# Kernel optimization log

Measured on AMD Instinct MI355X. Metric: run time of the kernel, lower is better.

## Reference

```python
import jax, jax.numpy as jnp
import numpy as np

N_HEAD = 16
TEMPERATURE = 1.0

def setup_inputs() -> dict:
    key = jax.random.key(0)
    ks = jax.random.split(key, 5)
    B, L, D = 2, 2048, 1024
    s = 0.02
    return {
        'x':     jax.random.normal(ks[0], (B, L, D), jnp.float32),
        'q_g':   jax.random.normal(ks[1], (B, L, D), jnp.float32),
        'k_g':   jax.random.normal(ks[2], (B, L, D), jnp.float32),
        'W_qkv': jax.random.normal(ks[3], (D, 3 * D), jnp.float32) * s,
        'W_out': jax.random.normal(ks[4], (D, D), jnp.float32) * s,
    }

def reference(x, q_g, k_g, W_qkv, W_out):
    B, L, D = x.shape
    H = N_HEAD
    hd = D // H
    qkv = x @ W_qkv                                    # [B, L, 3D]
    q, k, v = jnp.split(qkv, 3, axis=-1)
    def to_heads(t):                                    # [B,L,D] -> [B,H,L,hd]
        return t.reshape(B, L, H, hd).transpose(0, 2, 1, 3)
    q, k, v = to_heads(q), to_heads(k), to_heads(v)
    qg, kg = to_heads(q_g), to_heads(k_g)

    scale = 1.0 / jnp.sqrt(jnp.float32(hd))
    # dual score matrices (same math as concat-on-head-dim then split)
    aw_x = jnp.einsum('bhqd,bhkd->bhqk', q, k) * scale    # [B,H,L,L]
    aw_g = jnp.einsum('bhqd,bhkd->bhqk', qg, kg) * scale  # [B,H,L,L]
    # sensory_attention=True, merge='add'
    attn = aw_x + aw_g

    causal = jnp.tril(jnp.ones((L, L), dtype=bool))
    attn = jnp.where(causal, attn, -jnp.inf)
    log_norm = jnp.log(jnp.float32(L))                    # softmax_log_norm=True
    attn = jax.nn.softmax(attn / (log_norm * TEMPERATURE), axis=-1)

    y = jnp.einsum('bhqk,bhkd->bhqd', attn, v)            # [B,H,L,hd]
    y = y.transpose(0, 2, 1, 3).reshape(B, L, D)
    return y @ W_out
```

## Files before the change

### kernel.cpp

```cpp
#include <hip/hip_runtime.h>

typedef __attribute__((ext_vector_type(8))) short bf16x8;
typedef __attribute__((ext_vector_type(4))) float f32x4;

static __device__ __forceinline__ unsigned short f2bf(float f) {
    unsigned int u = __float_as_uint(f);
    u += 0x7fffu + ((u >> 16) & 1u);
    return (unsigned short)(u >> 16);
}
static __device__ __forceinline__ unsigned int pack2bf(float lo, float hi) {
    return ((__float_as_uint(lo) + 0x8000u) >> 16) |
           ((__float_as_uint(hi) + 0x8000u) & 0xffff0000u);
}
static __device__ __forceinline__ float bf2f(short v) {
    return __uint_as_float(((unsigned int)(unsigned short)v) << 16);
}
static __device__ __forceinline__ bf16x8 cvt8v(const float* p) {
    f32x4 a = *(const f32x4*)p, b = *(const f32x4*)(p + 4);
    bf16x8 r;
    r[0] = (short)f2bf(a[0]); r[1] = (short)f2bf(a[1]);
    r[2] = (short)f2bf(a[2]); r[3] = (short)f2bf(a[3]);
    r[4] = (short)f2bf(b[0]); r[5] = (short)f2bf(b[1]);
    r[6] = (short)f2bf(b[2]); r[7] = (short)f2bf(b[3]);
    return r;
}
static __device__ __forceinline__ bf16x8 scale8v(bf16x8 v, float s) {
    bf16x8 r;
    #pragma unroll
    for (int j = 0; j < 8; ++j) r[j] = (short)f2bf(bf2f(v[j]) * s);
    return r;
}
static __device__ __forceinline__ uint4 cvt8(const float* p) {
    bf16x8 r = cvt8v(p);
    union { bf16x8 v; uint4 u; } c; c.v = r; return c.u;
}
static __device__ __forceinline__ void glds16(const unsigned short* g, unsigned short* l) {
    __builtin_amdgcn_global_load_lds(
        (const __attribute__((address_space(1))) unsigned int*)g,
        (__attribute__((address_space(3))) unsigned int*)l, 16, 0, 0);
}

static __device__ __forceinline__ void transpose_tile(
    const float* __restrict__ src, unsigned short* __restrict__ dst,
    int R, int C, int bx, int by, int tid)
{
    __shared__ unsigned short t[64 * 72];
    const int r0 = by * 64, c0 = bx * 64;
    #pragma unroll
    for (int i = 0; i < 4; ++i) {
        int idx = tid + i * 256;
        int row = idx >> 4, seg = idx & 15;
        f32x4 v = *(const f32x4*)&src[(size_t)(r0 + row) * C + c0 + seg * 4];
        #pragma unroll
        for (int j = 0; j < 4; ++j) t[row * 72 + seg * 4 + j] = f2bf(v[j]);
    }
    __syncthreads();
    #pragma unroll
    for (int i = 0; i < 2; ++i) {
        int idx = tid + i * 256;
        int row = idx >> 3, seg = idx & 7;
        uint4 tv; unsigned short* tmp = (unsigned short*)&tv;
        #pragma unroll
        for (int j = 0; j < 8; ++j) tmp[j] = t[(seg * 8 + j) * 72 + row];
        *(uint4*)&dst[(size_t)(c0 + row) * R + r0 + seg * 8] = tv;
    }
}

__global__ __launch_bounds__(256) void prep_all(
    const float* __restrict__ x, unsigned short* __restrict__ x_bf,
    const float* __restrict__ kg, unsigned short* __restrict__ kg_bf,
    const float* __restrict__ Wq, unsigned short* __restrict__ wtq,
    const float* __restrict__ Wo, unsigned short* __restrict__ wto)
{
    const int t = blockIdx.x, tid = threadIdx.x;
    if (t < 2048) {
        size_t j = ((size_t)t * 256 + tid) * 8;
        *(uint4*)&x_bf[j] = cvt8(&x[j]);
    } else if (t < 4096) {
        size_t j = ((size_t)(t - 2048) * 256 + tid) * 8;
        *(uint4*)&kg_bf[j] = cvt8(&kg[j]);
    } else if (t < 4864) {
        int tt = t - 4096;
        transpose_tile(Wq, wtq, 1024, 3072, tt % 48, tt / 48, tid);
    } else {
        int tt = t - 4864;
        transpose_tile(Wo, wto, 1024, 1024, tt & 15, tt >> 4, tid);
    }
}

__global__ __launch_bounds__(256) void gemm_qkv(
    const unsigned short* __restrict__ A, const unsigned short* __restrict__ Bt,
    unsigned short* __restrict__ qk, unsigned short* __restrict__ vt)
{
    const int K = 1024;
    __shared__ unsigned short As[128 * 32];
    __shared__ unsigned short Bs[128 * 32];
    __shared__ unsigned short Tb[128 * 136];
    const int tid = threadIdx.x;
    const int wave = tid >> 6, lane = tid & 63, quad = lane >> 4, l16 = lane & 15;
    const int wr = (wave >> 1) * 64, wc = (wave & 1) * 64;
    const int m0 = blockIdx.y * 128, n0 = blockIdx.x * 128;

    const unsigned short* ga = A  + (size_t)(m0 + wave * 32 + (lane >> 2)) * K + (lane & 3) * 8;
    const unsigned short* gb = Bt + (size_t)(n0 + wave * 32 + (lane >> 2)) * K + (lane & 3) * 8;
    unsigned short* la = &As[wave * 32 * 32];
    unsigned short* lb = &Bs[wave * 32 * 32];
    const size_t step16 = (size_t)16 * K;

    f32x4 acc[4][4];
    #pragma unroll
    for (int i = 0; i < 4; ++i)
        #pragma unroll
        for (int j = 0; j < 4; ++j) acc[i][j] = (f32x4){0.f, 0.f, 0.f, 0.f};

    for (int kt = 0; kt < K; kt += 32) {
        glds16(ga, la); glds16(ga + step16, la + 512);
        glds16(gb, lb); glds16(gb + step16, lb + 512);
        ga += 32; gb += 32;
        __syncthreads();
        bf16x8 af[4], bf[4];
        #pragma unroll
        for (int i = 0; i < 4; ++i) {
            af[i] = *(const bf16x8*)&As[(wr + i * 16 + l16) * 32 + quad * 8];
            bf[i] = *(const bf16x8*)&Bs[(wc + i * 16 + l16) * 32 + quad * 8];
        }
        #pragma unroll
        for (int mi = 0; mi < 4; ++mi)
            #pragma unroll
            for (int ni = 0; ni < 4; ++ni)
                acc[mi][ni] = __builtin_amdgcn_mfma_f32_16x16x32_bf16(
                    af[mi], bf[ni], acc[mi][ni], 0, 0, 0);
        __syncthreads();
    }

    if (blockIdx.x < 16) {
        #pragma unroll
        for (int mi = 0; mi < 4; ++mi)
            #pragma unroll
            for (int ni = 0; ni < 4; ++ni)
                #pragma unroll
                for (int r = 0; r < 4; ++r) {
                    int row = m0 + wr + mi * 16 + quad * 4 + r;
                    int col = n0 + wc + ni * 16 + l16;
                    qk[(size_t)row * 2048 + col] = f2bf(acc[mi][ni][r]);
                }
    } else {
        __syncthreads();
        #pragma unroll
        for (int mi = 0; mi < 4; ++mi)
            #pragma unroll
            for (int ni = 0; ni < 4; ++ni)
                #pragma unroll
                for (int r = 0; r < 4; ++r) {
                    int col = wc + ni * 16 + l16;
                    int row = wr + mi * 16 + quad * 4 + r;
                    Tb[col * 136 + row] = f2bf(acc[mi][ni][r]);
                }
        __syncthreads();
        const int col = tid >> 1, r0 = (tid & 1) * 64;
        const int bh = (m0 >> 11) * 16 + ((int)blockIdx.x - 16) * 2 + (col >> 6);
        size_t base = ((size_t)bh * 64 + (col & 63)) * 2048 + (m0 & 2047) + r0;
        #pragma unroll
        for (int k = 0; k < 8; ++k)
            *(uint4*)&vt[base + k * 8] = *(const uint4*)&Tb[col * 136 + r0 + k * 8];
    }
}

__global__ __launch_bounds__(256) void gemm_n64(
    const unsigned short* __restrict__ A, const unsigned short* __restrict__ Bt,
    float* __restrict__ C)
{
    const int K = 1024, N = 1024;
    __shared__ unsigned short As[128 * 32];
    __shared__ unsigned short Bs[64 * 32];
    const int tid = threadIdx.x;
    const int wave = tid >> 6, lane = tid & 63, quad = lane >> 4, l16 = lane & 15;
    const int wr = (wave >> 1) * 64, wc = (wave & 1) * 32;
    const int m0 = blockIdx.y * 128, n0 = blockIdx.x * 64;

    const unsigned short* ga = A  + (size_t)(m0 + wave * 32 + (lane >> 2)) * K + (lane & 3) * 8;
    const unsigned short* gb = Bt + (size_t)(n0 + wave * 16 + (lane >> 2)) * K + (lane & 3) * 8;
    unsigned short* la = &As[wave * 32 * 32];
    unsigned short* lb = &Bs[wave * 16 * 32];
    const size_t step16 = (size_t)16 * K;

    f32x4 acc[4][2];
    #pragma unroll
    for (int i = 0; i < 4; ++i)
        #pragma unroll
        for (int j = 0; j < 2; ++j) acc[i][j] = (f32x4){0.f, 0.f, 0.f, 0.f};

    for (int kt = 0; kt < K; kt += 32) {
        glds16(ga, la); glds16(ga + step16, la + 512);
        glds16(gb, lb);
        ga += 32; gb += 32;
        __syncthreads();
        bf16x8 af[4], bf[2];
        #pragma unroll
        for (int i = 0; i < 4; ++i)
            af[i] = *(const bf16x8*)&As[(wr + i * 16 + l16) * 32 + quad * 8];
        #pragma unroll
        for (int i = 0; i < 2; ++i)
            bf[i] = *(const bf16x8*)&Bs[(wc + i * 16 + l16) * 32 + quad * 8];
        #pragma unroll
        for (int mi = 0; mi < 4; ++mi)
            #pragma unroll
            for (int ni = 0; ni < 2; ++ni)
                acc[mi][ni] = __builtin_amdgcn_mfma_f32_16x16x32_bf16(
                    af[mi], bf[ni], acc[mi][ni], 0, 0, 0);
        __syncthreads();
    }
    #pragma unroll
    for (int mi = 0; mi < 4; ++mi)
        #pragma unroll
        for (int ni = 0; ni < 2; ++ni)
            #pragma unroll
            for (int r = 0; r < 4; ++r) {
                int row = m0 + wr + mi * 16 + quad * 4 + r;
                int col = n0 + wc + ni * 16 + l16;
                C[(size_t)row * N + col] = acc[mi][ni][r];
            }
}

__global__ __launch_bounds__(256, 5) void attn7(
    const unsigned short* __restrict__ qk, const float* __restrict__ qg,
    const unsigned short* __restrict__ kgb, const unsigned short* __restrict__ vt,
    unsigned short* __restrict__ y)
{
    const int L = 2048, DS = 2048, Dm = 1024;
    const float SC2 = 0.125f * 1.44269504088896f / 7.6246189861593985f;

    const int qt = 31 - (int)blockIdx.y;
    const int bh = blockIdx.x, b = bh >> 4, h = bh & 15;
    const int tid = threadIdx.x, wave = tid >> 6, lane = tid & 63;
    const int quad = lane >> 4, l16 = lane & 15;

    __shared__ unsigned short K_l[4096];
    __shared__ unsigned short G_l[4096];
    __shared__ unsigned short V_l[4096];
    __shared__ unsigned short P_l[4096];
    unsigned short* Pw = &P_l[wave * 1024];

    bf16x8 qf[2], gf[2];
    {
        const int qrow = qt * 64 + wave * 16 + l16;
        const unsigned short* qp = qk + (size_t)(b * L + qrow) * DS + h * 64;
        const float* gp = qg + (size_t)(b * L + qrow) * Dm + h * 64;
        #pragma unroll
        for (int c = 0; c < 2; ++c) {
            qf[c] = scale8v(*(const bf16x8*)(qp + c * 32 + quad * 8), SC2);
            gf[c] = scale8v(cvt8v(gp + c * 32 + quad * 8), SC2);
        }
    }

    f32x4 o[4];
    #pragma unroll
    for (int nd = 0; nd < 4; ++nd) o[nd] = (f32x4){0.f, 0.f, 0.f, 0.f};
    float lsum = 0.f;

    const int srow = wave * 16 + (lane >> 3);
    const int c8 = (((lane & 7) ^ (lane >> 3)) & 7) * 8;
    const unsigned short* pk = qk + (size_t)(b * L + srow) * DS + 1024 + h * 64 + c8;
    const unsigned short* pg = kgb + (size_t)(b * L + srow) * Dm + h * 64 + c8;
    const unsigned short* pv = vt + ((size_t)bh * 64 + srow) * L + c8;
    unsigned short* lK = &K_l[wave * 1024];
    unsigned short* lG = &G_l[wave * 1024];
    unsigned short* lV = &V_l[wave * 1024];

    const int rb = l16 * 128;
    const int swz0 = ((quad     ^ (l16 & 7)) * 16);
    const int swz1 = (((4 + quad) ^ (l16 & 7)) * 16);
    const int pwb = l16 * 64 + (quad & 1) * 4;
    const int pwc = quad >> 1, pxr = l16 & 7;

    for (int kt = 0; kt < qt; ++kt) {
        __syncthreads();
        glds16(pk, lK); glds16(pk + 8 * DS, lK + 512);
        glds16(pg, lG); glds16(pg + 8 * Dm, lG + 512);
        glds16(pv, lV); glds16(pv + 8 * L,  lV + 512);
        pk += 64 * DS; pg += 64 * Dm; pv += 64;
        __syncthreads();

        #pragma unroll
        for (int ni = 0; ni < 4; ++ni) {
            bf16x8 kf0 = *(const bf16x8*)((const char*)K_l + rb + swz0 + ni * 2048);
            bf16x8 kf1 = *(const bf16x8*)((const char*)K_l + rb + swz1 + ni * 2048);
            bf16x8 gb0 = *(const bf16x8*)((const char*)G_l + rb + swz0 + ni * 2048);
            bf16x8 gb1 = *(const bf16x8*)((const char*)G_l + rb + swz1 + ni * 2048);
            f32x4 a = (f32x4){0.f, 0.f, 0.f, 0.f};
            a = __builtin_amdgcn_mfma_f32_16x16x32_bf16(kf0, qf[0], a, 0, 0, 0);
            a = __builtin_amdgcn_mfma_f32_16x16x32_bf16(gb0, gf[0], a, 0, 0, 0);
            a = __builtin_amdgcn_mfma_f32_16x16x32_bf16(kf1, qf[1], a, 0, 0, 0);
            a = __builtin_amdgcn_mfma_f32_16x16x32_bf16(gb1, gf[1], a, 0, 0, 0);
            float e0 = exp2f(a[0]), e1 = exp2f(a[1]);
            float e2 = exp2f(a[2]), e3 = exp2f(a[3]);
            lsum += (e0 + e1) + (e2 + e3);
            unsigned int p01 = pack2bf(e0, e1), p23 = pack2bf(e2, e3);
            *(unsigned long long*)&Pw[pwb + (((ni * 2 + pwc) ^ pxr) * 8)] =
                ((unsigned long long)p23 << 32) | p01;
        }
        asm volatile("s_waitcnt lgkmcnt(0)" ::: "memory");

        bf16x8 pa[2];
        #pragma unroll
        for (int c = 0; c < 2; ++c)
            pa[c] = *(const bf16x8*)&Pw[l16 * 64 + (((c * 4 + quad) ^ pxr) * 8)];
        #pragma unroll
        for (int nd = 0; nd < 4; ++nd) {
            bf16x8 vf0 = *(const bf16x8*)((const char*)V_l + rb + swz0 + nd * 2048);
            bf16x8 vf1 = *(const bf16x8*)((const char*)V_l + rb + swz1 + nd * 2048);
            o[nd] = __builtin_amdgcn_mfma_f32_16x16x32_bf16(pa[0], vf0, o[nd], 0, 0, 0);
            o[nd] = __builtin_amdgcn_mfma_f32_16x16x32_bf16(pa[1], vf1, o[nd], 0, 0, 0);
        }
    }

    {
        __syncthreads();
        glds16(pk, lK); glds16(pk + 8 * DS, lK + 512);
        glds16(pg, lG); glds16(pg + 8 * Dm, lG + 512);
        glds16(pv, lV); glds16(pv + 8 * L,  lV + 512);
        __syncthreads();

        #pragma unroll
        for (int ni = 0; ni < 4; ++ni) {
            if (ni > wave) {
                *(unsigned long long*)&Pw[pwb + (((ni * 2 + pwc) ^ pxr) * 8)] = 0ull;
                continue;
            }
            bf16x8 kf0 = *(const bf16x8*)((const char*)K_l + rb + swz0 + ni * 2048);
            bf16x8 kf1 = *(const bf16x8*)((const char*)K_l + rb + swz1 + ni * 2048);
            bf16x8 gb0 = *(const bf16x8*)((const char*)G_l + rb + swz0 + ni * 2048);
            bf16x8 gb1 = *(const bf16x8*)((const char*)G_l + rb + swz1 + ni * 2048);
            f32x4 a = (f32x4){0.f, 0.f, 0.f, 0.f};
            a = __builtin_amdgcn_mfma_f32_16x16x32_bf16(kf0, qf[0], a, 0, 0, 0);
            a = __builtin_amdgcn_mfma_f32_16x16x32_bf16(gb0, gf[0], a, 0, 0, 0);
            a = __builtin_amdgcn_mfma_f32_16x16x32_bf16(kf1, qf[1], a, 0, 0, 0);
            a = __builtin_amdgcn_mfma_f32_16x16x32_bf16(gb1, gf[1], a, 0, 0, 0);
            float e0, e1, e2, e3;
            if (ni < wave) {
                e0 = exp2f(a[0]); e1 = exp2f(a[1]);
                e2 = exp2f(a[2]); e3 = exp2f(a[3]);
            } else {
                e0 = (quad * 4 + 0 <= l16) ? exp2f(a[0]) : 0.f;
                e1 = (quad * 4 + 1 <= l16) ? exp2f(a[1]) : 0.f;
                e2 = (quad * 4 + 2 <= l16) ? exp2f(a[2]) : 0.f;
                e3 = (quad * 4 + 3 <= l16) ? exp2f(a[3]) : 0.f;
            }
            lsum += (e0 + e1) + (e2 + e3);
            unsigned int p01 = pack2bf(e0, e1), p23 = pack2bf(e2, e3);
            *(unsigned long long*)&Pw[pwb + (((ni * 2 + pwc) ^ pxr) * 8)] =
                ((unsigned long long)p23 << 32) | p01;
        }
        asm volatile("s_waitcnt lgkmcnt(0)" ::: "memory");

        bf16x8 pa[2];
        #pragma unroll
        for (int c = 0; c < 2; ++c)
            pa[c] = *(const bf16x8*)&Pw[l16 * 64 + (((c * 4 + quad) ^ pxr) * 8)];
        #pragma unroll
        for (int nd = 0; nd < 4; ++nd) {
            bf16x8 vf0 = *(const bf16x8*)((const char*)V_l + rb + swz0 + nd * 2048);
            bf16x8 vf1 = *(const bf16x8*)((const char*)V_l + rb + swz1 + nd * 2048);
            o[nd] = __builtin_amdgcn_mfma_f32_16x16x32_bf16(pa[0], vf0, o[nd], 0, 0, 0);
            o[nd] = __builtin_amdgcn_mfma_f32_16x16x32_bf16(pa[1], vf1, o[nd], 0, 0, 0);
        }
    }

    float rs = lsum;
    rs += __shfl_xor(rs, 16);
    rs += __shfl_xor(rs, 32);
    #pragma unroll
    for (int r = 0; r < 4; ++r) {
        float inv = 1.f / __shfl(rs, (lane & 48) | (quad * 4 + r));
        int row = qt * 64 + wave * 16 + quad * 4 + r;
        #pragma unroll
        for (int nd = 0; nd < 4; ++nd)
            y[(size_t)(b * L + row) * Dm + h * 64 + nd * 16 + l16] =
                f2bf(o[nd][r] * inv);
    }
}

extern "C" void kernel_launch(void* const* d_in, const int* in_sizes, int n_in,
                              void* d_out, int out_size, void* d_ws, size_t ws_size,
                              hipStream_t stream) {
    const float* x     = (const float*)d_in[0];
    const float* q_g   = (const float*)d_in[1];
    const float* k_g   = (const float*)d_in[2];
    const float* W_qkv = (const float*)d_in[3];
    const float* W_out = (const float*)d_in[4];
    float* out = (float*)d_out;
    unsigned short* ws = (unsigned short*)d_ws;

    unsigned short* qk_ws = ws;
    unsigned short* y_ws  = ws + 8388608;
    unsigned short* wtq   = ws + 12582912;
    unsigned short* wto   = ws + 15728640;
    unsigned short* kg_bf = ws + 16777216;
    unsigned short* x_bf  = ws + 20971520;
    unsigned short* vt_bf = ws + 25165824;

    dim3 blk(256);
    prep_all<<<5120, blk, 0, stream>>>(x, x_bf, k_g, kg_bf, W_qkv, wtq, W_out, wto);
    gemm_qkv<<<dim3(24, 32), blk, 0, stream>>>(x_bf, wtq, qk_ws, vt_bf);
    attn7<<<dim3(32, 32), blk, 0, stream>>>(qk_ws, q_g, kg_bf, vt_bf, y_ws);
    gemm_n64<<<dim3(16, 32), blk, 0, stream>>>(y_ws, wto, out);
}
```

Measured before the change: 225.1 us.

## Double-buffer K/G/V tiles and widen attention query tile to 128 rows

Result: slower. 240.1 us (+6.7%).

```diff
diff --git a/kernel.cpp b/kernel.cpp
--- a/kernel.cpp
+++ b/kernel.cpp
@@ -222,7 +222,84 @@
             }
 }
 
-__global__ __launch_bounds__(256, 5) void attn7(
+template<bool DIAG>
+static __device__ __forceinline__ void attn_tile(
+    const unsigned short* __restrict__ Kc, const unsigned short* __restrict__ Gc,
+    const unsigned short* __restrict__ Vc, unsigned short* __restrict__ Pw,
+    const bf16x8 (&qf)[2][2], const bf16x8 (&gf)[2][2],
+    f32x4 (&o)[2][4], float (&lsum)[2],
+    int rb, int swz0, int swz1, int pxr, int quad, int l16, int wave, int reld)
+{
+    auto pstore = [&](int qj, int ni, unsigned long long v) {
+        *(unsigned long long*)&Pw[(qj * 16 + l16) * 64 + (quad & 1) * 4 +
+                                  (((ni * 2 + (quad >> 1)) ^ pxr) * 8)] = v;
+    };
+
+    #pragma unroll
+    for (int ni = 0; ni < 4; ++ni) {
+        const int kbase = (DIAG ? reld * 64 : 0) + ni * 16;
+        if (DIAG && kbase > wave * 32 + 31) {
+            pstore(0, ni, 0ull); pstore(1, ni, 0ull);
+            continue;
+        }
+        bf16x8 kf0 = *(const bf16x8*)((const char*)Kc + rb + swz0 + ni * 2048);
+        bf16x8 kf1 = *(const bf16x8*)((const char*)Kc + rb + swz1 + ni * 2048);
+        bf16x8 gb0 = *(const bf16x8*)((const char*)Gc + rb + swz0 + ni * 2048);
+        bf16x8 gb1 = *(const bf16x8*)((const char*)Gc + rb + swz1 + ni * 2048);
+        #pragma unroll
+        for (int qj = 0; qj < 2; ++qj) {
+            const int qtop = wave * 32 + qj * 16;
+            if (DIAG && kbase > qtop + 15) {
+                pstore(qj, ni, 0ull);
+                continue;
+            }
+            f32x4 a = (f32x4){0.f, 0.f, 0.f, 0.f};
+            a = __builtin_amdgcn_mfma_f32_16x16x32_bf16(kf0, qf[qj][0], a, 0, 0, 0);
+            a = __builtin_amdgcn_mfma_f32_16x16x32_bf16(gb0, gf[qj][0], a, 0, 0, 0);
+            a = __builtin_amdgcn_mfma_f32_16x16x32_bf16(kf1, qf[qj][1], a, 0, 0, 0);
+            a = __builtin_amdgcn_mfma_f32_16x16x32_bf16(gb1, gf[qj][1], a, 0, 0, 0);
+            float e0, e1, e2, e3;
+            if (DIAG && (kbase + 15 > qtop)) {
+                const int qr = qtop + l16, kb = kbase + quad * 4;
+                e0 = (kb + 0 <= qr) ? exp2f(a[0]) : 0.f;
+                e1 = (kb + 1 <= qr) ? exp2f(a[1]) : 0.f;
+                e2 = (kb + 2 <= qr) ? exp2f(a[2]) : 0.f;
+                e3 = (kb + 3 <= qr) ? exp2f(a[3]) : 0.f;
+            } else {
+                e0 = exp2f(a[0]); e1 = exp2f(a[1]);
+                e2 = exp2f(a[2]); e3 = exp2f(a[3]);
+            }
+            lsum[qj] += (e0 + e1) + (e2 + e3);
+            unsigned int p01 = pack2bf(e0, e1), p23 = pack2bf(e2, e3);
+            pstore(qj, ni, ((unsigned long long)p23 << 32) | p01);
+        }
+    }
+
+    bf16x8 vf[4][2];
+    #pragma unroll
+    for (int nd = 0; nd < 4; ++nd) {
+        vf[nd][0] = *(const bf16x8*)((const char*)Vc + rb + swz0 + nd * 2048);
+        vf[nd][1] = *(const bf16x8*)((const char*)Vc + rb + swz1 + nd * 2048);
+    }
+    asm volatile("s_waitcnt lgkmcnt(0)" ::: "memory");
+
+    bf16x8 pa[2][2];
+    #pragma unroll
+    for (int qj = 0; qj < 2; ++qj)
+        #pragma unroll
+        for (int c = 0; c < 2; ++c)
+            pa[qj][c] = *(const bf16x8*)&Pw[(qj * 16 + l16) * 64 +
+                                            (((c * 4 + quad) ^ pxr) * 8)];
+    #pragma unroll
+    for (int nd = 0; nd < 4; ++nd) {
+        o[0][nd] = __builtin_amdgcn_mfma_f32_16x16x32_bf16(pa[0][0], vf[nd][0], o[0][nd], 0, 0, 0);
+        o[0][nd] = __builtin_amdgcn_mfma_f32_16x16x32_bf16(pa[0][1], vf[nd][1], o[0][nd], 0, 0, 0);
+        o[1][nd] = __builtin_amdgcn_mfma_f32_16x16x32_bf16(pa[1][0], vf[nd][0], o[1][nd], 0, 0, 0);
+        o[1][nd] = __builtin_amdgcn_mfma_f32_16x16x32_bf16(pa[1][1], vf[nd][1], o[1][nd], 0, 0, 0);
+    }
+}
+
+__global__ __launch_bounds__(256, 2) void attn8(
     const unsigned short* __restrict__ qk, const float* __restrict__ qg,
     const unsigned short* __restrict__ kgb, const unsigned short* __restrict__ vt,
     unsigned short* __restrict__ y)
@@ -230,153 +307,96 @@
     const int L = 2048, DS = 2048, Dm = 1024;
     const float SC2 = 0.125f * 1.44269504088896f / 7.6246189861593985f;
 
-    const int qt = 31 - (int)blockIdx.y;
+    const int yb = (int)blockIdx.y;
+    const int qt = (yb < 8) ? (15 - yb) : (yb - 8);
     const int bh = blockIdx.x, b = bh >> 4, h = bh & 15;
     const int tid = threadIdx.x, wave = tid >> 6, lane = tid & 63;
     const int quad = lane >> 4, l16 = lane & 15;
 
-    __shared__ unsigned short K_l[4096];
-    __shared__ unsigned short G_l[4096];
-    __shared__ unsigned short V_l[4096];
-    __shared__ unsigned short P_l[4096];
-    unsigned short* Pw = &P_l[wave * 1024];
-
-    bf16x8 qf[2], gf[2];
-    {
-        const int qrow = qt * 64 + wave * 16 + l16;
-        const unsigned short* qp = qk + (size_t)(b * L + qrow) * DS + h * 64;
-        const float* gp = qg + (size_t)(b * L + qrow) * Dm + h * 64;
+    __shared__ unsigned short K_l[2][4096];
+    __shared__ unsigned short G_l[2][4096];
+    __shared__ unsigned short V_l[2][4096];
+    __shared__ unsigned short P_l[8192];
+    unsigned short* Pw = &P_l[wave * 2048];
+
+    bf16x8 qf[2][2], gf[2][2];
+    const int qrow0 = qt * 128 + wave * 32;
+    #pragma unroll
+    for (int qj = 0; qj < 2; ++qj) {
+        const unsigned short* qp = qk + (size_t)(b * L + qrow0 + qj * 16 + l16) * DS + h * 64;
+        const float* gp = qg + (size_t)(b * L + qrow0 + qj * 16 + l16) * Dm + h * 64;
         #pragma unroll
         for (int c = 0; c < 2; ++c) {
-            qf[c] = scale8v(*(const bf16x8*)(qp + c * 32 + quad * 8), SC2);
-            gf[c] = scale8v(cvt8v(gp + c * 32 + quad * 8), SC2);
+            qf[qj][c] = scale8v(*(const bf16x8*)(qp + c * 32 + quad * 8), SC2);
+            gf[qj][c] = scale8v(cvt8v(gp + c * 32 + quad * 8), SC2);
         }
     }
 
-    f32x4 o[4];
-    #pragma unroll
-    for (int nd = 0; nd < 4; ++nd) o[nd] = (f32x4){0.f, 0.f, 0.f, 0.f};
-    float lsum = 0.f;
+    f32x4 o[2][4];
+    #pragma unroll
+    for (int qj = 0; qj < 2; ++qj)
+        #pragma unroll
+        for (int nd = 0; nd < 4; ++nd) o[qj][nd] = (f32x4){0.f, 0.f, 0.f, 0.f};
+    float lsum[2] = {0.f, 0.f};
 
     const int srow = wave * 16 + (lane >> 3);
     const int c8 = (((lane & 7) ^ (lane >> 3)) & 7) * 8;
     const unsigned short* pk = qk + (size_t)(b * L + srow) * DS + 1024 + h * 64 + c8;
     const unsigned short* pg = kgb + (size_t)(b * L + srow) * Dm + h * 64 + c8;
     const unsigned short* pv = vt + ((size_t)bh * 64 + srow) * L + c8;
-    unsigned short* lK = &K_l[wave * 1024];
-    unsigned short* lG = &G_l[wave * 1024];
-    unsigned short* lV = &V_l[wave * 1024];
-
-    const int rb = l16 * 128;
-    const int swz0 = ((quad     ^ (l16 & 7)) * 16);
-    const int swz1 = (((4 + quad) ^ (l16 & 7)) * 16);
-    const int pwb = l16 * 64 + (quad & 1) * 4;
-    const int pwc = quad >> 1, pxr = l16 & 7;
-
-    for (int kt = 0; kt < qt; ++kt) {
-        __syncthreads();
+
+    auto STAGE = [&](int bi) {
+        unsigned short* lK = &K_l[bi][wave * 1024];
+        unsigned short* lG = &G_l[bi][wave * 1024];
+        unsigned short* lV = &V_l[bi][wave * 1024];
         glds16(pk, lK); glds16(pk + 8 * DS, lK + 512);
         glds16(pg, lG); glds16(pg + 8 * Dm, lG + 512);
         glds16(pv, lV); glds16(pv + 8 * L,  lV + 512);
         pk += 64 * DS; pg += 64 * Dm; pv += 64;
-        __syncthreads();
-
-        #pragma unroll
-        for (int ni = 0; ni < 4; ++ni) {
-            bf16x8 kf0 = *(const bf16x8*)((const char*)K_l + rb + swz0 + ni * 2048);
-            bf16x8 kf1 = *(const bf16x8*)((const char*)K_l + rb + swz1 + ni * 2048);
-            bf16x8 gb0 = *(const bf16x8*)((const char*)G_l + rb + swz0 + ni * 2048);
-            bf16x8 gb1 = *(const bf16x8*)((const char*)G_l + rb + swz1 + ni * 2048);
-            f32x4 a = (f32x4){0.f, 0.f, 0.f, 0.f};
-            a = __builtin_amdgcn_mfma_f32_16x16x32_bf16(kf0, qf[0], a, 0, 0, 0);
-            a = __builtin_amdgcn_mfma_f32_16x16x32_bf16(gb0, gf[0], a, 0, 0, 0);
-            a = __builtin_amdgcn_mfma_f32_16x16x32_bf16(kf1, qf[1], a, 0, 0, 0);
-            a = __builtin_amdgcn_mfma_f32_16x16x32_bf16(gb1, gf[1], a, 0, 0, 0);
-            float e0 = exp2f(a[0]), e1 = exp2f(a[1]);
-            float e2 = exp2f(a[2]), e3 = exp2f(a[3]);
-            lsum += (e0 + e1) + (e2 + e3);
-            unsigned int p01 = pack2bf(e0, e1), p23 = pack2bf(e2, e3);
-            *(unsigned long long*)&Pw[pwb + (((ni * 2 + pwc) ^ pxr) * 8)] =
-                ((unsigned long long)p23 << 32) | p01;
+    };
+
+    const int rb = l16 * 128;
+    const int swz0 = ((quad ^ (l16 & 7)) * 16);
+    const int swz1 = (((4 + quad) ^ (l16 & 7)) * 16);
+    const int pxr = l16 & 7;
+
+    STAGE(0);
+    int cur = 0;
+
+    for (int kt = 0; kt < 2 * qt; ++kt) {
+        asm volatile("s_waitcnt vmcnt(0)" ::: "memory");
+        __syncthreads();
+        STAGE(cur ^ 1);
+        attn_tile<false>(&K_l[cur][0], &G_l[cur][0], &V_l[cur][0], Pw,
+                         qf, gf, o, lsum, rb, swz0, swz1, pxr, quad, l16, wave, 0);
+        cur ^= 1;
+    }
+
+    #pragma unroll
+    for (int d = 0; d < 2; ++d) {
+        asm volatile("s_waitcnt vmcnt(0)" ::: "memory");
+        __syncthreads();
+        if (d == 0) STAGE(cur ^ 1);
+        if (!(d == 1 && wave < 2))
+            attn_tile<true>(&K_l[cur][0], &G_l[cur][0], &V_l[cur][0], Pw,
+                            qf, gf, o, lsum, rb, swz0, swz1, pxr, quad, l16, wave, d);
+        cur ^= 1;
+    }
+
+    #pragma unroll
+    for (int qj = 0; qj < 2; ++qj) {
+        float rs = lsum[qj];
+        rs += __shfl_xor(rs, 16);
+        rs += __shfl_xor(rs, 32);
+        #pragma unroll
+        for (int r = 0; r < 4; ++r) {
+            float inv = 1.f / __shfl(rs, (lane & 48) | (quad * 4 + r));
+            int row = qt * 128 + wave * 32 + qj * 16 + quad * 4 + r;
+            #pragma unroll
+            for (int nd = 0; nd < 4; ++nd)
+                y[(size_t)(b * L + row) * Dm + h * 64 + nd * 16 + l16] =
+                    f2bf(o[qj][nd][r] * inv);
         }
-        asm volatile("s_waitcnt lgkmcnt(0)" ::: "memory");
-
-        bf16x8 pa[2];
-        #pragma unroll
-        for (int c = 0; c < 2; ++c)
-            pa[c] = *(const bf16x8*)&Pw[l16 * 64 + (((c * 4 + quad) ^ pxr) * 8)];
-        #pragma unroll
-        for (int nd = 0; nd < 4; ++nd) {
-            bf16x8 vf0 = *(const bf16x8*)((const char*)V_l + rb + swz0 + nd * 2048);
-            bf16x8 vf1 = *(const bf16x8*)((const char*)V_l + rb + swz1 + nd * 2048);
-            o[nd] = __builtin_amdgcn_mfma_f32_16x16x32_bf16(pa[0], vf0, o[nd], 0, 0, 0);
-            o[nd] = __builtin_amdgcn_mfma_f32_16x16x32_bf16(pa[1], vf1, o[nd], 0, 0, 0);
-        }
-    }
-
-    {
-        __syncthreads();
-        glds16(pk, lK); glds16(pk + 8 * DS, lK + 512);
-        glds16(pg, lG); glds16(pg + 8 * Dm, lG + 512);
-        glds16(pv, lV); glds16(pv + 8 * L,  lV + 512);
-        __syncthreads();
-
-        #pragma unroll
-        for (int ni = 0; ni < 4; ++ni) {
-            if (ni > wave) {
-                *(unsigned long long*)&Pw[pwb + (((ni * 2 + pwc) ^ pxr) * 8)] = 0ull;
-                continue;
-            }
-            bf16x8 kf0 = *(const bf16x8*)((const char*)K_l + rb + swz0 + ni * 2048);
-            bf16x8 kf1 = *(const bf16x8*)((const char*)K_l + rb + swz1 + ni * 2048);
-            bf16x8 gb0 = *(const bf16x8*)((const char*)G_l + rb + swz0 + ni * 2048);
-            bf16x8 gb1 = *(const bf16x8*)((const char*)G_l + rb + swz1 + ni * 2048);
-            f32x4 a = (f32x4){0.f, 0.f, 0.f, 0.f};
-            a = __builtin_amdgcn_mfma_f32_16x16x32_bf16(kf0, qf[0], a, 0, 0, 0);
-            a = __builtin_amdgcn_mfma_f32_16x16x32_bf16(gb0, gf[0], a, 0, 0, 0);
-            a = __builtin_amdgcn_mfma_f32_16x16x32_bf16(kf1, qf[1], a, 0, 0, 0);
-            a = __builtin_amdgcn_mfma_f32_16x16x32_bf16(gb1, gf[1], a, 0, 0, 0);
-            float e0, e1, e2, e3;
-            if (ni < wave) {
-                e0 = exp2f(a[0]); e1 = exp2f(a[1]);
-                e2 = exp2f(a[2]); e3 = exp2f(a[3]);
-            } else {
-                e0 = (quad * 4 + 0 <= l16) ? exp2f(a[0]) : 0.f;
-                e1 = (quad * 4 + 1 <= l16) ? exp2f(a[1]) : 0.f;
-                e2 = (quad * 4 + 2 <= l16) ? exp2f(a[2]) : 0.f;
-                e3 = (quad * 4 + 3 <= l16) ? exp2f(a[3]) : 0.f;
-            }
-            lsum += (e0 + e1) + (e2 + e3);
-            unsigned int p01 = pack2bf(e0, e1), p23 = pack2bf(e2, e3);
-            *(unsigned long long*)&Pw[pwb + (((ni * 2 + pwc) ^ pxr) * 8)] =
-                ((unsigned long long)p23 << 32) | p01;
-        }
-        asm volatile("s_waitcnt lgkmcnt(0)" ::: "memory");
-
-        bf16x8 pa[2];
-        #pragma unroll
-        for (int c = 0; c < 2; ++c)
-            pa[c] = *(const bf16x8*)&Pw[l16 * 64 + (((c * 4 + quad) ^ pxr) * 8)];
-        #pragma unroll
-        for (int nd = 0; nd < 4; ++nd) {
-            bf16x8 vf0 = *(const bf16x8*)((const char*)V_l + rb + swz0 + nd * 2048);
-            bf16x8 vf1 = *(const bf16x8*)((const char*)V_l + rb + swz1 + nd * 2048);
-            o[nd] = __builtin_amdgcn_mfma_f32_16x16x32_bf16(pa[0], vf0, o[nd], 0, 0, 0);
-            o[nd] = __builtin_amdgcn_mfma_f32_16x16x32_bf16(pa[1], vf1, o[nd], 0, 0, 0);
-        }
-    }
-
-    float rs = lsum;
-    rs += __shfl_xor(rs, 16);
-    rs += __shfl_xor(rs, 32);
-    #pragma unroll
-    for (int r = 0; r < 4; ++r) {
-        float inv = 1.f / __shfl(rs, (lane & 48) | (quad * 4 + r));
-        int row = qt * 64 + wave * 16 + quad * 4 + r;
-        #pragma unroll
-        for (int nd = 0; nd < 4; ++nd)
-            y[(size_t)(b * L + row) * Dm + h * 64 + nd * 16 + l16] =
-                f2bf(o[nd][r] * inv);
     }
 }
 
@@ -402,6 +422,6 @@
     dim3 blk(256);
     prep_all<<<5120, blk, 0, stream>>>(x, x_bf, k_g, kg_bf, W_qkv, wtq, W_out, wto);
     gemm_qkv<<<dim3(24, 32), blk, 0, stream>>>(x_bf, wtq, qk_ws, vt_bf);
-    attn7<<<dim3(32, 32), blk, 0, stream>>>(qk_ws, q_g, kg_bf, vt_bf, y_ws);
+    attn8<<<dim3(32, 16), blk, 0, stream>>>(qk_ws, q_g, kg_bf, vt_bf, y_ws);
     gemm_n64<<<dim3(16, 32), blk, 0, stream>>>(y_ws, wto, out);
 }
```

## Double-buffer K/G/V LDS tiles in attention to overlap loads with compute

Applied to the files above, without the earlier changes.

After: 236.7 us. +5.1%, slower.

```diff
diff --git a/kernel.cpp b/kernel.cpp
--- a/kernel.cpp
+++ b/kernel.cpp
@@ -222,7 +222,66 @@
             }
 }
 
-__global__ __launch_bounds__(256, 5) void attn7(
+template<bool DIAG>
+static __device__ __forceinline__ void attn_tile(
+    const unsigned short* __restrict__ Kc, const unsigned short* __restrict__ Gc,
+    const unsigned short* __restrict__ Vc, unsigned short* __restrict__ Pw,
+    const bf16x8 (&qf)[2], const bf16x8 (&gf)[2],
+    f32x4 (&o)[4], float& lsum,
+    int rb, int swz0, int swz1, int pxr, int quad, int l16, int wave,
+    int pwb, int pwc)
+{
+    #pragma unroll
+    for (int ni = 0; ni < 4; ++ni) {
+        if (DIAG && ni > wave) {
+            *(unsigned long long*)&Pw[pwb + (((ni * 2 + pwc) ^ pxr) * 8)] = 0ull;
+            continue;
+        }
+        bf16x8 kf0 = *(const bf16x8*)((const char*)Kc + rb + swz0 + ni * 2048);
+        bf16x8 kf1 = *(const bf16x8*)((const char*)Kc + rb + swz1 + ni * 2048);
+        bf16x8 gb0 = *(const bf16x8*)((const char*)Gc + rb + swz0 + ni * 2048);
+        bf16x8 gb1 = *(const bf16x8*)((const char*)Gc + rb + swz1 + ni * 2048);
+        f32x4 a = (f32x4){0.f, 0.f, 0.f, 0.f};
+        a = __builtin_amdgcn_mfma_f32_16x16x32_bf16(kf0, qf[0], a, 0, 0, 0);
+        a = __builtin_amdgcn_mfma_f32_16x16x32_bf16(gb0, gf[0], a, 0, 0, 0);
+        a = __builtin_amdgcn_mfma_f32_16x16x32_bf16(kf1, qf[1], a, 0, 0, 0);
+        a = __builtin_amdgcn_mfma_f32_16x16x32_bf16(gb1, gf[1], a, 0, 0, 0);
+        float e0, e1, e2, e3;
+        if (DIAG && ni == wave) {
+            e0 = (quad * 4 + 0 <= l16) ? exp2f(a[0]) : 0.f;
+            e1 = (quad * 4 + 1 <= l16) ? exp2f(a[1]) : 0.f;
+            e2 = (quad * 4 + 2 <= l16) ? exp2f(a[2]) : 0.f;
+            e3 = (quad * 4 + 3 <= l16) ? exp2f(a[3]) : 0.f;
+        } else {
+            e0 = exp2f(a[0]); e1 = exp2f(a[1]);
+            e2 = exp2f(a[2]); e3 = exp2f(a[3]);
+        }
+        lsum += (e0 + e1) + (e2 + e3);
+        unsigned int p01 = pack2bf(e0, e1), p23 = pack2bf(e2, e3);
+        *(unsigned long long*)&Pw[pwb + (((ni * 2 + pwc) ^ pxr) * 8)] =
+            ((unsigned long long)p23 << 32) | p01;
+    }
+
+    bf16x8 vf[4][2];
+    #pragma unroll
+    for (int nd = 0; nd < 4; ++nd) {
+        vf[nd][0] = *(const bf16x8*)((const char*)Vc + rb + swz0 + nd * 2048);
+        vf[nd][1] = *(const bf16x8*)((const char*)Vc + rb + swz1 + nd * 2048);
+    }
+    asm volatile("s_waitcnt lgkmcnt(0)" ::: "memory");
+
+    bf16x8 pa[2];
+    #pragma unroll
+    for (int c = 0; c < 2; ++c)
+        pa[c] = *(const bf16x8*)&Pw[l16 * 64 + (((c * 4 + quad) ^ pxr) * 8)];
+    #pragma unroll
+    for (int nd = 0; nd < 4; ++nd) {
+        o[nd] = __builtin_amdgcn_mfma_f32_16x16x32_bf16(pa[0], vf[nd][0], o[nd], 0, 0, 0);
+        o[nd] = __builtin_amdgcn_mfma_f32_16x16x32_bf16(pa[1], vf[nd][1], o[nd], 0, 0, 0);
+    }
+}
+
+__global__ __launch_bounds__(256, 3) void attn10(
     const unsigned short* __restrict__ qk, const float* __restrict__ qg,
     const unsigned short* __restrict__ kgb, const unsigned short* __restrict__ vt,
     unsigned short* __restrict__ y)
@@ -235,9 +294,9 @@
     const int tid = threadIdx.x, wave = tid >> 6, lane = tid & 63;
     const int quad = lane >> 4, l16 = lane & 15;
 
-    __shared__ unsigned short K_l[4096];
-    __shared__ unsigned short G_l[4096];
-    __shared__ unsigned short V_l[4096];
+    __shared__ unsigned short K_l[2][4096];
+    __shared__ unsigned short G_l[2][4096];
+    __shared__ unsigned short V_l[2][4096];
     __shared__ unsigned short P_l[4096];
     unsigned short* Pw = &P_l[wave * 1024];
 
@@ -263,9 +322,16 @@
     const unsigned short* pk = qk + (size_t)(b * L + srow) * DS + 1024 + h * 64 + c8;
     const unsigned short* pg = kgb + (size_t)(b * L + srow) * Dm + h * 64 + c8;
     const unsigned short* pv = vt + ((size_t)bh * 64 + srow) * L + c8;
-    unsigned short* lK = &K_l[wave * 1024];
-    unsigned short* lG = &G_l[wave * 1024];
-    unsigned short* lV = &V_l[wave * 1024];
+
+    auto STAGE = [&](int bi) {
+        unsigned short* lK = &K_l[bi][wave * 1024];
+        unsigned short* lG = &G_l[bi][wave * 1024];
+        unsigned short* lV = &V_l[bi][wave * 1024];
+        glds16(pk, lK); glds16(pk + 8 * DS, lK + 512);
+        glds16(pg, lG); glds16(pg + 8 * Dm, lG + 512);
+        glds16(pv, lV); glds16(pv + 8 * L,  lV + 512);
+        pk += 64 * DS; pg += 64 * Dm; pv += 64;
+    };
 
     const int rb = l16 * 128;
     const int swz0 = ((quad     ^ (l16 & 7)) * 16);
@@ -273,97 +339,23 @@
     const int pwb = l16 * 64 + (quad & 1) * 4;
     const int pwc = quad >> 1, pxr = l16 & 7;
 
+    STAGE(0);
+    int cur = 0;
+
     for (int kt = 0; kt < qt; ++kt) {
         __syncthreads();
-        glds16(pk, lK); glds16(pk + 8 * DS, lK + 512);
-        glds16(pg, lG); glds16(pg + 8 * Dm, lG + 512);
-        glds16(pv, lV); glds16(pv + 8 * L,  lV + 512);
-        pk += 64 * DS; pg += 64 * Dm; pv += 64;
-        __syncthreads();
-
-        #pragma unroll
-        for (int ni = 0; ni < 4; ++ni) {
-            bf16x8 kf0 = *(const bf16x8*)((const char*)K_l + rb + swz0 + ni * 2048);
-            bf16x8 kf1 = *(const bf16x8*)((const char*)K_l + rb + swz1 + ni * 2048);
-            bf16x8 gb0 = *(const bf16x8*)((const char*)G_l + rb + swz0 + ni * 2048);
-            bf16x8 gb1 = *(const bf16x8*)((const char*)G_l + rb + swz1 + ni * 2048);
-            f32x4 a = (f32x4){0.f, 0.f, 0.f, 0.f};
-            a = __builtin_amdgcn_mfma_f32_16x16x32_bf16(kf0, qf[0], a, 0, 0, 0);
-            a = __builtin_amdgcn_mfma_f32_16x16x32_bf16(gb0, gf[0], a, 0, 0, 0);
-            a = __builtin_amdgcn_mfma_f32_16x16x32_bf16(kf1, qf[1], a, 0, 0, 0);
-            a = __builtin_amdgcn_mfma_f32_16x16x32_bf16(gb1, gf[1], a, 0, 0, 0);
-            float e0 = exp2f(a[0]), e1 = exp2f(a[1]);
-            float e2 = exp2f(a[2]), e3 = exp2f(a[3]);
-            lsum += (e0 + e1) + (e2 + e3);
-            unsigned int p01 = pack2bf(e0, e1), p23 = pack2bf(e2, e3);
-            *(unsigned long long*)&Pw[pwb + (((ni * 2 + pwc) ^ pxr) * 8)] =
-                ((unsigned long long)p23 << 32) | p01;
-        }
-        asm volatile("s_waitcnt lgkmcnt(0)" ::: "memory");
-
-        bf16x8 pa[2];
-        #pragma unroll
-        for (int c = 0; c < 2; ++c)
-            pa[c] = *(const bf16x8*)&Pw[l16 * 64 + (((c * 4 + quad) ^ pxr) * 8)];
-        #pragma unroll
-        for (int nd = 0; nd < 4; ++nd) {
-            bf16x8 vf0 = *(const bf16x8*)((const char*)V_l + rb + swz0 + nd * 2048);
-            bf16x8 vf1 = *(const bf16x8*)((const char*)V_l + rb + swz1 + nd * 2048);
-            o[nd] = __builtin_amdgcn_mfma_f32_16x16x32_bf16(pa[0], vf0, o[nd], 0, 0, 0);
-            o[nd] = __builtin_amdgcn_mfma_f32_16x16x32_bf16(pa[1], vf1, o[nd], 0, 0, 0);
-        }
+        STAGE(cur ^ 1);
+        attn_tile<false>(&K_l[cur][0], &G_l[cur][0], &V_l[cur][0], Pw,
+                         qf, gf, o, lsum, rb, swz0, swz1, pxr, quad, l16, wave,
+                         pwb, pwc);
+        cur ^= 1;
     }
 
     {
         __syncthreads();
-        glds16(pk, lK); glds16(pk + 8 * DS, lK + 512);
-        glds16(pg, lG); glds16(pg + 8 * Dm, lG + 512);
-        glds16(pv, lV); glds16(pv + 8 * L,  lV + 512);
-        __syncthreads();
-
-        #pragma unroll
-        for (int ni = 0; ni < 4; ++ni) {
-            if (ni > wave) {
-                *(unsigned long long*)&Pw[pwb + (((ni * 2 + pwc) ^ pxr) * 8)] = 0ull;
-                continue;
-            }
-            bf16x8 kf0 = *(const bf16x8*)((const char*)K_l + rb + swz0 + ni * 2048);
-            bf16x8 kf1 = *(const bf16x8*)((const char*)K_l + rb + swz1 + ni * 2048);
-            bf16x8 gb0 = *(const bf16x8*)((const char*)G_l + rb + swz0 + ni * 2048);
-            bf16x8 gb1 = *(const bf16x8*)((const char*)G_l + rb + swz1 + ni * 2048);
-            f32x4 a = (f32x4){0.f, 0.f, 0.f, 0.f};
-            a = __builtin_amdgcn_mfma_f32_16x16x32_bf16(kf0, qf[0], a, 0, 0, 0);
-            a = __builtin_amdgcn_mfma_f32_16x16x32_bf16(gb0, gf[0], a, 0, 0, 0);
-            a = __builtin_amdgcn_mfma_f32_16x16x32_bf16(kf1, qf[1], a, 0, 0, 0);
-            a = __builtin_amdgcn_mfma_f32_16x16x32_bf16(gb1, gf[1], a, 0, 0, 0);
-            float e0, e1, e2, e3;
-            if (ni < wave) {
-                e0 = exp2f(a[0]); e1 = exp2f(a[1]);
-                e2 = exp2f(a[2]); e3 = exp2f(a[3]);
-            } else {
-                e0 = (quad * 4 + 0 <= l16) ? exp2f(a[0]) : 0.f;
-                e1 = (quad * 4 + 1 <= l16) ? exp2f(a[1]) : 0.f;
-                e2 = (quad * 4 + 2 <= l16) ? exp2f(a[2]) : 0.f;
-                e3 = (quad * 4 + 3 <= l16) ? exp2f(a[3]) : 0.f;
-            }
-            lsum += (e0 + e1) + (e2 + e3);
-            unsigned int p01 = pack2bf(e0, e1), p23 = pack2bf(e2, e3);
-            *(unsigned long long*)&Pw[pwb + (((ni * 2 + pwc) ^ pxr) * 8)] =
-                ((unsigned long long)p23 << 32) | p01;
-        }
-        asm volatile("s_waitcnt lgkmcnt(0)" ::: "memory");
-
-        bf16x8 pa[2];
-        #pragma unroll
-        for (int c = 0; c < 2; ++c)
-            pa[c] = *(const bf16x8*)&Pw[l16 * 64 + (((c * 4 + quad) ^ pxr) * 8)];
-        #pragma unroll
-        for (int nd = 0; nd < 4; ++nd) {
-            bf16x8 vf0 = *(const bf16x8*)((const char*)V_l + rb + swz0 + nd * 2048);
-            bf16x8 vf1 = *(const bf16x8*)((const char*)V_l + rb + swz1 + nd * 2048);
-            o[nd] = __builtin_amdgcn_mfma_f32_16x16x32_bf16(pa[0], vf0, o[nd], 0, 0, 0);
-            o[nd] = __builtin_amdgcn_mfma_f32_16x16x32_bf16(pa[1], vf1, o[nd], 0, 0, 0);
-        }
+        attn_tile<true>(&K_l[cur][0], &G_l[cur][0], &V_l[cur][0], Pw,
+                        qf, gf, o, lsum, rb, swz0, swz1, pxr, quad, l16, wave,
+                        pwb, pwc);
     }
 
     float rs = lsum;
@@ -402,6 +394,6 @@
     dim3 blk(256);
     prep_all<<<5120, blk, 0, stream>>>(x, x_bf, k_g, kg_bf, W_qkv, wtq, W_out, wto);
     gemm_qkv<<<dim3(24, 32), blk, 0, stream>>>(x_bf, wtq, qk_ws, vt_bf);
-    attn7<<<dim3(32, 32), blk, 0, stream>>>(qk_ws, q_g, kg_bf, vt_bf, y_ws);
+    attn10<<<dim3(32, 32), blk, 0, stream>>>(qk_ws, q_g, kg_bf, vt_bf, y_ws);
     gemm_n64<<<dim3(16, 32), blk, 0, stream>>>(y_ws, wto, out);
 }
```

## Deepen GEMM K-tile to 64, remap blocks by XCD, shrink output GEMM tile

Applied to the files above, without the earlier changes.

Measured after the change: 228.8 us. No clear change (+1.6%).

```diff
diff --git a/kernel.cpp b/kernel.cpp
--- a/kernel.cpp
+++ b/kernel.cpp
@@ -93,19 +93,24 @@
     unsigned short* __restrict__ qk, unsigned short* __restrict__ vt)
 {
     const int K = 1024;
-    __shared__ unsigned short As[128 * 32];
-    __shared__ unsigned short Bs[128 * 32];
-    __shared__ unsigned short Tb[128 * 136];
+    __shared__ unsigned short U[128 * 136];
+    unsigned short* As = U;
+    unsigned short* Bs = U + 8192;
+    unsigned short* Tb = U;
     const int tid = threadIdx.x;
     const int wave = tid >> 6, lane = tid & 63, quad = lane >> 4, l16 = lane & 15;
     const int wr = (wave >> 1) * 64, wc = (wave & 1) * 64;
-    const int m0 = blockIdx.y * 128, n0 = blockIdx.x * 128;
-
-    const unsigned short* ga = A  + (size_t)(m0 + wave * 32 + (lane >> 2)) * K + (lane & 3) * 8;
-    const unsigned short* gb = Bt + (size_t)(n0 + wave * 32 + (lane >> 2)) * K + (lane & 3) * 8;
-    unsigned short* la = &As[wave * 32 * 32];
-    unsigned short* lb = &Bs[wave * 32 * 32];
-    const size_t step16 = (size_t)16 * K;
+
+    const int lin = (int)blockIdx.y * 24 + (int)blockIdx.x;
+    const int wl = (lin & 7) * 96 + (lin >> 3);
+    const int wx = wl % 24, wy = wl / 24;
+    const int m0 = wy * 128, n0 = wx * 128;
+
+    const unsigned short* ga = A  + (size_t)(m0 + wave * 32 + (lane >> 3)) * K + (lane & 7) * 8;
+    const unsigned short* gb = Bt + (size_t)(n0 + wave * 32 + (lane >> 3)) * K + (lane & 7) * 8;
+    unsigned short* la = As + wave * 32 * 64;
+    unsigned short* lb = Bs + wave * 32 * 64;
+    const size_t step8 = (size_t)8 * K;
 
     f32x4 acc[4][4];
     #pragma unroll
@@ -113,27 +118,33 @@
         #pragma unroll
         for (int j = 0; j < 4; ++j) acc[i][j] = (f32x4){0.f, 0.f, 0.f, 0.f};
 
-    for (int kt = 0; kt < K; kt += 32) {
-        glds16(ga, la); glds16(ga + step16, la + 512);
-        glds16(gb, lb); glds16(gb + step16, lb + 512);
-        ga += 32; gb += 32;
-        __syncthreads();
-        bf16x8 af[4], bf[4];
-        #pragma unroll
-        for (int i = 0; i < 4; ++i) {
-            af[i] = *(const bf16x8*)&As[(wr + i * 16 + l16) * 32 + quad * 8];
-            bf[i] = *(const bf16x8*)&Bs[(wc + i * 16 + l16) * 32 + quad * 8];
-        }
-        #pragma unroll
-        for (int mi = 0; mi < 4; ++mi)
-            #pragma unroll
-            for (int ni = 0; ni < 4; ++ni)
-                acc[mi][ni] = __builtin_amdgcn_mfma_f32_16x16x32_bf16(
-                    af[mi], bf[ni], acc[mi][ni], 0, 0, 0);
-        __syncthreads();
-    }
-
-    if (blockIdx.x < 16) {
+    for (int kt = 0; kt < K; kt += 64) {
+        #pragma unroll
+        for (int g = 0; g < 4; ++g) {
+            glds16(ga + g * step8, la + g * 512);
+            glds16(gb + g * step8, lb + g * 512);
+        }
+        ga += 64; gb += 64;
+        __syncthreads();
+        #pragma unroll
+        for (int h = 0; h < 2; ++h) {
+            bf16x8 af[4], bf[4];
+            #pragma unroll
+            for (int i = 0; i < 4; ++i) {
+                af[i] = *(const bf16x8*)&As[(wr + i * 16 + l16) * 64 + h * 32 + quad * 8];
+                bf[i] = *(const bf16x8*)&Bs[(wc + i * 16 + l16) * 64 + h * 32 + quad * 8];
+            }
+            #pragma unroll
+            for (int mi = 0; mi < 4; ++mi)
+                #pragma unroll
+                for (int ni = 0; ni < 4; ++ni)
+                    acc[mi][ni] = __builtin_amdgcn_mfma_f32_16x16x32_bf16(
+                        af[mi], bf[ni], acc[mi][ni], 0, 0, 0);
+        }
+        __syncthreads();
+    }
+
+    if (wx < 16) {
         #pragma unroll
         for (int mi = 0; mi < 4; ++mi)
             #pragma unroll
@@ -158,7 +169,7 @@
                 }
         __syncthreads();
         const int col = tid >> 1, r0 = (tid & 1) * 64;
-        const int bh = (m0 >> 11) * 16 + ((int)blockIdx.x - 16) * 2 + (col >> 6);
+        const int bh = (m0 >> 11) * 16 + (wx - 16) * 2 + (col >> 6);
         size_t base = ((size_t)bh * 64 + (col & 63)) * 2048 + (m0 & 2047) + r0;
         #pragma unroll
         for (int k = 0; k < 8; ++k)
@@ -171,47 +182,53 @@
     float* __restrict__ C)
 {
     const int K = 1024, N = 1024;
-    __shared__ unsigned short As[128 * 32];
-    __shared__ unsigned short Bs[64 * 32];
+    __shared__ unsigned short As[64 * 64];
+    __shared__ unsigned short Bs[64 * 64];
     const int tid = threadIdx.x;
     const int wave = tid >> 6, lane = tid & 63, quad = lane >> 4, l16 = lane & 15;
-    const int wr = (wave >> 1) * 64, wc = (wave & 1) * 32;
-    const int m0 = blockIdx.y * 128, n0 = blockIdx.x * 64;
-
-    const unsigned short* ga = A  + (size_t)(m0 + wave * 32 + (lane >> 2)) * K + (lane & 3) * 8;
-    const unsigned short* gb = Bt + (size_t)(n0 + wave * 16 + (lane >> 2)) * K + (lane & 3) * 8;
-    unsigned short* la = &As[wave * 32 * 32];
-    unsigned short* lb = &Bs[wave * 16 * 32];
-    const size_t step16 = (size_t)16 * K;
-
-    f32x4 acc[4][2];
-    #pragma unroll
-    for (int i = 0; i < 4; ++i)
+    const int wr = (wave >> 1) * 32, wc = (wave & 1) * 32;
+
+    const int lin = (int)blockIdx.y * 16 + (int)blockIdx.x;
+    const int wl = (lin & 7) * 128 + (lin >> 3);
+    const int wx = wl & 15, wy = wl >> 4;
+    const int m0 = wy * 64, n0 = wx * 64;
+
+    const unsigned short* ga = A  + (size_t)(m0 + wave * 16 + (lane >> 3)) * K + (lane & 7) * 8;
+    const unsigned short* gb = Bt + (size_t)(n0 + wave * 16 + (lane >> 3)) * K + (lane & 7) * 8;
+    unsigned short* la = &As[wave * 16 * 64];
+    unsigned short* lb = &Bs[wave * 16 * 64];
+    const size_t step8 = (size_t)8 * K;
+
+    f32x4 acc[2][2];
+    #pragma unroll
+    for (int i = 0; i < 2; ++i)
         #pragma unroll
         for (int j = 0; j < 2; ++j) acc[i][j] = (f32x4){0.f, 0.f, 0.f, 0.f};
 
-    for (int kt = 0; kt < K; kt += 32) {
-        glds16(ga, la); glds16(ga + step16, la + 512);
-        glds16(gb, lb);
-        ga += 32; gb += 32;
-        __syncthreads();
-        bf16x8 af[4], bf[2];
-        #pragma unroll
-        for (int i = 0; i < 4; ++i)
-            af[i] = *(const bf16x8*)&As[(wr + i * 16 + l16) * 32 + quad * 8];
-        #pragma unroll
-        for (int i = 0; i < 2; ++i)
-            bf[i] = *(const bf16x8*)&Bs[(wc + i * 16 + l16) * 32 + quad * 8];
-        #pragma unroll
-        for (int mi = 0; mi < 4; ++mi)
-            #pragma unroll
-            for (int ni = 0; ni < 2; ++ni)
-                acc[mi][ni] = __builtin_amdgcn_mfma_f32_16x16x32_bf16(
-                    af[mi], bf[ni], acc[mi][ni], 0, 0, 0);
-        __syncthreads();
-    }
-    #pragma unroll
-    for (int mi = 0; mi < 4; ++mi)
+    for (int kt = 0; kt < K; kt += 64) {
+        glds16(ga, la); glds16(ga + step8, la + 512);
+        glds16(gb, lb); glds16(gb + step8, lb + 512);
+        ga += 64; gb += 64;
+        __syncthreads();
+        #pragma unroll
+        for (int h = 0; h < 2; ++h) {
+            bf16x8 af[2], bf[2];
+            #pragma unroll
+            for (int i = 0; i < 2; ++i) {
+                af[i] = *(const bf16x8*)&As[(wr + i * 16 + l16) * 64 + h * 32 + quad * 8];
+                bf[i] = *(const bf16x8*)&Bs[(wc + i * 16 + l16) * 64 + h * 32 + quad * 8];
+            }
+            #pragma unroll
+            for (int mi = 0; mi < 2; ++mi)
+                #pragma unroll
+                for (int ni = 0; ni < 2; ++ni)
+                    acc[mi][ni] = __builtin_amdgcn_mfma_f32_16x16x32_bf16(
+                        af[mi], bf[ni], acc[mi][ni], 0, 0, 0);
+        }
+        __syncthreads();
+    }
+    #pragma unroll
+    for (int mi = 0; mi < 2; ++mi)
         #pragma unroll
         for (int ni = 0; ni < 2; ++ni)
             #pragma unroll
@@ -403,5 +420,5 @@
     prep_all<<<5120, blk, 0, stream>>>(x, x_bf, k_g, kg_bf, W_qkv, wtq, W_out, wto);
     gemm_qkv<<<dim3(24, 32), blk, 0, stream>>>(x_bf, wtq, qk_ws, vt_bf);
     attn7<<<dim3(32, 32), blk, 0, stream>>>(qk_ws, q_g, kg_bf, vt_bf, y_ws);
-    gemm_n64<<<dim3(16, 32), blk, 0, stream>>>(y_ws, wto, out);
-}
+    gemm_n64<<<dim3(16, 64), blk, 0, stream>>>(y_ws, wto, out);
+}
```
